# Kernel tuning notes

Measured on AMD Instinct MI355X. Metric: run time of the kernel, lower is better.

Reference implementation:

```python
import jax, jax.numpy as jnp
import numpy as np

B, S, H = 4, 4096, 1024
GAMMA = 0.96875


def decay_mask(seq_len, gamma, dtype=jnp.float32):
    # D[i, j] = gamma**(i-j) for i >= j, else 0 (causal gamma-decay mask)
    i = jnp.arange(seq_len)[:, None]
    j = jnp.arange(seq_len)[None, :]
    exp = (i - j).astype(dtype)
    return jnp.where(i >= j, jnp.power(jnp.asarray(gamma, dtype), exp), jnp.zeros((), dtype))


def setup_inputs() -> dict:
    key = jax.random.key(0)
    ks = jax.random.split(key, 6)
    sc = 1.0 / np.sqrt(H)
    return {
        "x": jax.random.normal(ks[0], (B, S, H), dtype=jnp.float32),
        "Wq": jax.random.normal(ks[1], (H, H), dtype=jnp.float32) * sc,
        "bq": jax.random.normal(ks[2], (H,), dtype=jnp.float32) * 0.01,
        "Wk": jax.random.normal(ks[3], (H, H), dtype=jnp.float32) * sc,
        "bk": jax.random.normal(ks[4], (H,), dtype=jnp.float32) * 0.01,
        "Wv": jax.random.normal(ks[5], (H, H), dtype=jnp.float32) * sc,
    }


def reference(x, Wq, bq, Wk, bk, Wv):
    # Parallel representation of retention.
    seq_len = x.shape[1]
    q = jnp.einsum("bsh,oh->bso", x, Wq) + bq  # [B,S,H]
    k = jnp.einsum("bsh,oh->bso", x, Wk) + bk  # [B,S,H]
    v = jnp.einsum("bsh,oh->bso", x, Wv)       # [B,S,H]
    D = decay_mask(seq_len, GAMMA, x.dtype)     # [S,S]
    scores = jnp.einsum("bqh,bkh->bqk", q, k) * D[None]  # [B,S,S]
    return jnp.einsum("bqk,bkh->bqh", scores, v)
```

## Files before the change

kernel.cpp:

```cpp
#include <hip/hip_runtime.h>


typedef __attribute__((ext_vector_type(8))) short short8;
typedef __attribute__((ext_vector_type(4))) float floatx4;

#define MFMA(a, b, c) __builtin_amdgcn_mfma_f32_16x16x32_bf16((a), (b), (c), 0, 0, 0)

#define B_SZ   4
#define S_LEN  4096
#define H_DIM  1024
#define NROWS  (B_SZ * S_LEN)
#define HP     1088
#define WR     1152
#define LOG2G  (-0.045803690f)

__device__ __forceinline__ unsigned short f32_to_bf16_rn(float f) {
    unsigned int u = __float_as_uint(f);
    u += 0x7FFFu + ((u >> 16) & 1u);
    return (unsigned short)(u >> 16);
}

#define GLOAD_LDS16(gptr, lptr)                                                        \
    __builtin_amdgcn_global_load_lds((__attribute__((address_space(1))) void*)(gptr),  \
                                     (__attribute__((address_space(3))) void*)(lptr),  \
                                     16, 0, 0)

__device__ __forceinline__ void cvt_bf16_body(int i, const float* __restrict__ src,
                                              unsigned short* __restrict__ dst, int n4) {
    if (i >= n4) return;
    float4 v = ((const float4*)src)[i];
    ushort4 o;
    o.x = f32_to_bf16_rn(v.x);
    o.y = f32_to_bf16_rn(v.y);
    o.z = f32_to_bf16_rn(v.z);
    o.w = f32_to_bf16_rn(v.w);
    ((ushort4*)dst)[i] = o;
}

__device__ __forceinline__ void cvt_x_body(int idx, const float* __restrict__ src,
                                           unsigned short* __restrict__ dst) {
    int row = idx >> 7, c8 = (idx & 127) * 8;
    const float4* s = (const float4*)(src + (size_t)row * H_DIM + c8);
    float4 a = s[0], b = s[1];
    ushort4 o0, o1;
    o0.x = f32_to_bf16_rn(a.x); o0.y = f32_to_bf16_rn(a.y);
    o0.z = f32_to_bf16_rn(a.z); o0.w = f32_to_bf16_rn(a.w);
    o1.x = f32_to_bf16_rn(b.x); o1.y = f32_to_bf16_rn(b.y);
    o1.z = f32_to_bf16_rn(b.z); o1.w = f32_to_bf16_rn(b.w);
    ushort4* d = (ushort4*)(dst + (size_t)row * HP + c8);
    d[0] = o0; d[1] = o1;
}

__device__ __forceinline__ void fill_pad_body(int idx, unsigned short* __restrict__ dst) {
    int row = idx >> 3, c = idx & 7;
    uint4 v; v.x = (c == 0) ? 0x00003F80u : 0u; v.y = 0u; v.z = 0u; v.w = 0u;
    *(uint4*)(dst + (size_t)row * HP + 1024 + c * 8) = v;
}

__device__ __forceinline__ void tr_cvt_body(float (&Lt)[128][33],
                                            const float* __restrict__ Wsrc,
                                            const float* __restrict__ bias,
                                            unsigned short* __restrict__ dst,
                                            int bx, int by, int tid) {
    if (by >= 32) {
        if (bx != 0) return;
        const int h0 = by * 32;
#pragma unroll
        for (int i = 0; i < 128; ++i) {
            int idx = i * 256 + tid;
            int r = idx >> 10, cc = idx & 1023;
            int h = h0 + r;
            float v = (h == 1024) ? bias[cc] : 0.0f;
            dst[(size_t)h * 1024 + cc] = f32_to_bf16_rn(v);
        }
        return;
    }
    const int w0 = bx * 128, h0 = by * 32;
#pragma unroll
    for (int i = 0; i < 16; ++i) {
        int idx = i * 256 + tid;
        int r = idx >> 5, cc = idx & 31;
        Lt[r][cc] = Wsrc[(size_t)(w0 + r) * 1024 + h0 + cc];
    }
    __syncthreads();
#pragma unroll
    for (int i = 0; i < 16; ++i) {
        int idx = i * 256 + tid;
        int hh = idx >> 7, ww = idx & 127;
        dst[(size_t)(h0 + hh) * 1024 + w0 + ww] = f32_to_bf16_rn(Lt[ww][hh]);
    }
}

template <int MODE>
__device__ __forceinline__ void gemm_body(unsigned short (&As)[2][128 * 32],
                                          unsigned short (&Bs)[2][128 * 32],
                                          int bx, int by,
                                          const unsigned short* __restrict__ A, int lda,
                                          const unsigned short* __restrict__ W, int ldw,
                                          void* __restrict__ outp, int ldo, int K, int p0) {
    const int tid  = threadIdx.x;
    const int lane = tid & 63;
    const int w4   = tid >> 6;
    const int wm   = w4 >> 1, wn = w4 & 1;
    const int l15  = lane & 15;
    const int q8   = (lane >> 4) * 8;
    const int q4   = (lane >> 4) * 4;

    int aRow0 = 0, wRow0 = 0, kStart = 0;
    const unsigned short* Ap = A;
    const unsigned short* Wp = W;
    const int tT = by;
    const int tl = tT & 31;
    int jt = 0;

    if (MODE == 0) {
        aRow0 = by * 128; wRow0 = bx * 128;
    } else if (MODE == 1) {
        aRow0 = bx * 128; wRow0 = by * 128;
    } else if (MODE == 2) {
        jt = tl - 4 + bx;
        if (jt < 0) return;
        aRow0 = tT * 128;
        wRow0 = (tT >> 5) * S_LEN + jt * 128;
    } else {
        kStart = (tl < 4) ? (4 - tl) * 128 : 0;
        Ap = A + (size_t)tT * 128 * 640;
        Wp = W + (size_t)((tT >> 5) * H_DIM + bx * 128) * S_LEN + (ptrdiff_t)(tl - 4) * 128;
    }

    floatx4 acc[4][4];
#pragma unroll
    for (int i = 0; i < 4; ++i)
#pragma unroll
        for (int j = 0; j < 4; ++j) acc[i][j] = (floatx4)0.0f;

    for (int k0 = kStart; k0 < K; k0 += 64) {
        __syncthreads();
#pragma unroll
        for (int p = 0; p < 2; ++p) {
            const int c = p * 256 + tid;
            const unsigned short* gA = Ap + (size_t)(aRow0 + (c >> 2)) * lda + k0 + (c & 3) * 8;
            const unsigned short* gW = Wp + (size_t)(wRow0 + (c >> 2)) * ldw + k0 + (c & 3) * 8;
            char* dA0 = (char*)&As[0][0] + (size_t)(p * 256 + w4 * 64) * 16;
            char* dA1 = (char*)&As[1][0] + (size_t)(p * 256 + w4 * 64) * 16;
            char* dB0 = (char*)&Bs[0][0] + (size_t)(p * 256 + w4 * 64) * 16;
            char* dB1 = (char*)&Bs[1][0] + (size_t)(p * 256 + w4 * 64) * 16;
            GLOAD_LDS16(gA,      dA0);
            GLOAD_LDS16(gA + 32, dA1);
            GLOAD_LDS16(gW,      dB0);
            GLOAD_LDS16(gW + 32, dB1);
        }
        __syncthreads();

#pragma unroll
        for (int h = 0; h < 2; ++h) {
            short8 af[4], bf[4];
#pragma unroll
            for (int mt = 0; mt < 4; ++mt)
                af[mt] = *(const short8*)(&As[h][0] + (wm * 64 + mt * 16 + l15) * 32 + q8);
#pragma unroll
            for (int nt = 0; nt < 4; ++nt)
                bf[nt] = *(const short8*)(&Bs[h][0] + (wn * 64 + nt * 16 + l15) * 32 + q8);
#pragma unroll
            for (int mt = 0; mt < 4; ++mt)
#pragma unroll
                for (int nt = 0; nt < 4; ++nt)
                    acc[mt][nt] = MFMA(af[mt], bf[nt], acc[mt][nt]);
        }
    }

#pragma unroll
    for (int nt = 0; nt < 4; ++nt) {
        const int ol = wn * 64 + nt * 16 + l15;
#pragma unroll
        for (int mt = 0; mt < 4; ++mt) {
#pragma unroll
            for (int r = 0; r < 4; ++r) {
                const int nl = wm * 64 + mt * 16 + q4 + r;
                const float v = acc[mt][nt][r];
                if (MODE == 0) {
                    const int o = wRow0 + ol;
                    if (o < p0)
                        ((unsigned short*)outp)[(size_t)(aRow0 + nl) * ldo + o] = f32_to_bf16_rn(v);
                } else if (MODE == 1) {
                    const int s = wRow0 + ol;
                    const int hh = aRow0 + nl;
                    ((unsigned short*)outp)[((size_t)(s >> 12) * H_DIM + hh) * S_LEN + (s & (S_LEN - 1))] =
                        f32_to_bf16_rn(v);
                } else if (MODE == 2) {
                    const int d = (tl - jt) * 128 + nl - ol;
                    const float pv = (d >= 0) ? v * exp2f((float)d * LOG2G) : 0.0f;
                    ((unsigned short*)outp)[(size_t)tT * (128 * 640) + (size_t)nl * 640 +
                                            (size_t)bx * 128 + ol] = f32_to_bf16_rn(pv);
                } else {
                    ((float*)outp)[(size_t)(tT * 128 + nl) * H_DIM + bx * 128 + ol] = v;
                }
            }
        }
    }
}

__global__ __launch_bounds__(256) void prep_small(const float* __restrict__ Wq,
                                                  const float* __restrict__ bq,
                                                  const float* __restrict__ Wk,
                                                  const float* __restrict__ bk,
                                                  const float* __restrict__ Wv,
                                                  unsigned short* __restrict__ wqT,
                                                  unsigned short* __restrict__ wkT,
                                                  unsigned short* __restrict__ wvb,
                                                  unsigned short* __restrict__ xtb) {
    __shared__ float Lt[128][33];
    const int t = blockIdx.x, tid = threadIdx.x;
    if (t < 288) {
        tr_cvt_body(Lt, Wq, bq, wqT, t & 7, t >> 3, tid);
    } else if (t < 576) {
        const int t2 = t - 288;
        tr_cvt_body(Lt, Wk, bk, wkT, t2 & 7, t2 >> 3, tid);
    } else if (t < 1600) {
        cvt_bf16_body((t - 576) * 256 + tid, Wv, wvb, H_DIM * H_DIM / 4);
    } else {
        fill_pad_body((t - 1600) * 256 + tid, xtb);
    }
}

__global__ __launch_bounds__(256) void cvtx_p1(const float* __restrict__ x,
                                               unsigned short* __restrict__ xtb,
                                               const unsigned short* __restrict__ wkT,
                                               const unsigned short* __restrict__ wqT,
                                               unsigned short* __restrict__ p1) {
    __shared__ unsigned short As[2][128 * 32];
    __shared__ unsigned short Bs[2][128 * 32];
    const int t = blockIdx.x;
    if (t < 81) {
        gemm_body<0>(As, Bs, t % 9, t / 9, wkT, 1024, wqT, 1024, p1, HP, 1024, HP);
    } else {
        cvt_x_body((t - 81) * 256 + threadIdx.x, x, xtb);
    }
}

__global__ __launch_bounds__(256) void gemm_g(const unsigned short* __restrict__ xtb,
                                              const unsigned short* __restrict__ p1,
                                              unsigned short* __restrict__ gb) {
    __shared__ unsigned short As[2][128 * 32];
    __shared__ unsigned short Bs[2][128 * 32];
    const int bid = blockIdx.x;
    const int g = bid & 7, j = bid >> 3;
    gemm_body<0>(As, Bs, j % 9, g * 16 + j / 9, xtb, HP, p1, HP, gb, HP, HP, HP);
}

__global__ __launch_bounds__(256) void pb_vt(const unsigned short* __restrict__ gb,
                                             const unsigned short* __restrict__ xtb,
                                             const unsigned short* __restrict__ wvb,
                                             unsigned short* __restrict__ pb,
                                             unsigned short* __restrict__ vtb) {
    __shared__ unsigned short As[2][128 * 32];
    __shared__ unsigned short Bs[2][128 * 32];
    const int t = blockIdx.x;
    if (t < 640) {
        const int g = t & 7, j = t >> 3;
        gemm_body<2>(As, Bs, j % 5, g * 16 + j / 5, gb, HP, xtb, HP, pb, 640, HP, 0);
    } else {
        const int t2 = t - 640;
        const int g = t2 & 7, j = t2 >> 3;
        gemm_body<1>(As, Bs, j & 7, g * 16 + (j >> 3), wvb, 1024, xtb, HP, vtb, 0, 1024, 0);
    }
}

__global__ __launch_bounds__(256) void gemm_out(const unsigned short* __restrict__ pb,
                                                const unsigned short* __restrict__ vtb,
                                                float* __restrict__ out) {
    __shared__ unsigned short As[2][128 * 32];
    __shared__ unsigned short Bs[2][128 * 32];
    const int bid = blockIdx.x;
    const int g = bid & 7, j = bid >> 3;
    gemm_body<3>(As, Bs, j & 7, g * 16 + (j >> 3), pb, 640, vtb, S_LEN, out, H_DIM, 640, 0);
}

extern "C" void kernel_launch(void* const* d_in, const int* in_sizes, int n_in,
                              void* d_out, int out_size, void* d_ws, size_t ws_size,
                              hipStream_t stream) {
    (void)in_sizes; (void)n_in; (void)out_size; (void)ws_size;

    const float* x  = (const float*)d_in[0];
    const float* Wq = (const float*)d_in[1];
    const float* bq = (const float*)d_in[2];
    const float* Wk = (const float*)d_in[3];
    const float* bk = (const float*)d_in[4];
    const float* Wv = (const float*)d_in[5];
    float* out = (float*)d_out;

    unsigned short* xtb = (unsigned short*)d_ws;
    unsigned short* gb  = xtb + (size_t)NROWS * HP;
    unsigned short* vtb = gb  + (size_t)NROWS * HP;
    unsigned short* pb  = vtb + (size_t)NROWS * H_DIM;
    unsigned short* wqT = pb  + (size_t)128 * 128 * 640;
    unsigned short* wkT = wqT + (size_t)WR * H_DIM;
    unsigned short* p1  = wkT + (size_t)WR * H_DIM;
    unsigned short* wvb = p1  + (size_t)WR * HP;

    prep_small<<<2112, 256, 0, stream>>>(Wq, bq, Wk, bk, Wv, wqT, wkT, wvb, xtb);
    cvtx_p1<<<81 + 8192, 256, 0, stream>>>(x, xtb, wkT, wqT, p1);
    gemm_g<<<9 * 128, 256, 0, stream>>>(xtb, p1, gb);
    pb_vt<<<640 + 1024, 256, 0, stream>>>(gb, xtb, wvb, pb, vtb);
    gemm_out<<<8 * 128, 256, 0, stream>>>(pb, vtb, out);
}
```

Baseline: 304.3 us.

## Switch main GEMMs to 256x256 tiles with 4-stage async LDS pipeline

Replaces the 128x128 tiles with 256-thread blocks in the three large GEMM stages by 256x256 tiles with 512-thread blocks. Each K step is staged through a 4-deep ring of global-to-LDS async loads using explicit vmcnt waits and barriers, with an XOR swizzle on LDS chunks and raised priority around the MFMA loops. The banded decay-score buffer is re-laid out for 256-wide tiles (768 columns), and unused parts of it are zeroed in the prep kernel. The larger tiles are meant to raise data reuse and hide memory latency. In exchange there are fewer blocks, higher register and LDS pressure, and more wasted work on the causal band.

```diff
diff --git a/kernel.cpp b/kernel.cpp
--- a/kernel.cpp
+++ b/kernel.cpp
@@ -11,7 +11,6 @@
 #define H_DIM  1024
 #define NROWS  (B_SZ * S_LEN)
 #define HP     1088
-#define WR     1152
 #define LOG2G  (-0.045803690f)
 
 __device__ __forceinline__ unsigned short f32_to_bf16_rn(float f) {
@@ -24,6 +23,13 @@
     __builtin_amdgcn_global_load_lds((__attribute__((address_space(1))) void*)(gptr),  \
                                      (__attribute__((address_space(3))) void*)(lptr),  \
                                      16, 0, 0)
+
+#define BAR()                                   \
+    do {                                        \
+        asm volatile("" ::: "memory");          \
+        __builtin_amdgcn_s_barrier();           \
+        asm volatile("" ::: "memory");          \
+    } while (0)
 
 __device__ __forceinline__ void cvt_bf16_body(int i, const float* __restrict__ src,
                                               unsigned short* __restrict__ dst, int n4) {
@@ -57,6 +63,17 @@
     *(uint4*)(dst + (size_t)row * HP + 1024 + c * 8) = v;
 }
 
+__device__ __forceinline__ void zero_pb_body(int idx, unsigned short* __restrict__ pb) {
+    int r = idx >> 13;
+    int rem = idx & 8191;
+    int row = rem >> 5, c8 = (rem & 31) * 8;
+    int batch = r / 3, sub = r % 3;
+    int qt = batch * 16 + (sub == 2 ? 1 : 0);
+    int col0 = (sub == 2 ? 0 : sub * 256);
+    uint4 z; z.x = 0u; z.y = 0u; z.z = 0u; z.w = 0u;
+    *(uint4*)(pb + (size_t)qt * (256 * 768) + (size_t)row * 768 + col0 + c8) = z;
+}
+
 __device__ __forceinline__ void tr_cvt_body(float (&Lt)[128][33],
                                             const float* __restrict__ Wsrc,
                                             const float* __restrict__ bias,
@@ -91,13 +108,13 @@
     }
 }
 
-template <int MODE>
-__device__ __forceinline__ void gemm_body(unsigned short (&As)[2][128 * 32],
-                                          unsigned short (&Bs)[2][128 * 32],
-                                          int bx, int by,
-                                          const unsigned short* __restrict__ A, int lda,
-                                          const unsigned short* __restrict__ W, int ldw,
-                                          void* __restrict__ outp, int ldo, int K, int p0) {
+__device__ __forceinline__ void gemm_body128(unsigned short (&As)[2][128 * 32],
+                                             unsigned short (&Bs)[2][128 * 32],
+                                             int bx, int by,
+                                             const unsigned short* __restrict__ A, int lda,
+                                             const unsigned short* __restrict__ W, int ldw,
+                                             unsigned short* __restrict__ outp, int ldo,
+                                             int K, int p0) {
     const int tid  = threadIdx.x;
     const int lane = tid & 63;
     const int w4   = tid >> 6;
@@ -106,27 +123,7 @@
     const int q8   = (lane >> 4) * 8;
     const int q4   = (lane >> 4) * 4;
 
-    int aRow0 = 0, wRow0 = 0, kStart = 0;
-    const unsigned short* Ap = A;
-    const unsigned short* Wp = W;
-    const int tT = by;
-    const int tl = tT & 31;
-    int jt = 0;
-
-    if (MODE == 0) {
-        aRow0 = by * 128; wRow0 = bx * 128;
-    } else if (MODE == 1) {
-        aRow0 = bx * 128; wRow0 = by * 128;
-    } else if (MODE == 2) {
-        jt = tl - 4 + bx;
-        if (jt < 0) return;
-        aRow0 = tT * 128;
-        wRow0 = (tT >> 5) * S_LEN + jt * 128;
-    } else {
-        kStart = (tl < 4) ? (4 - tl) * 128 : 0;
-        Ap = A + (size_t)tT * 128 * 640;
-        Wp = W + (size_t)((tT >> 5) * H_DIM + bx * 128) * S_LEN + (ptrdiff_t)(tl - 4) * 128;
-    }
+    const int aRow0 = by * 128, wRow0 = bx * 128;
 
     floatx4 acc[4][4];
 #pragma unroll
@@ -134,13 +131,13 @@
 #pragma unroll
         for (int j = 0; j < 4; ++j) acc[i][j] = (floatx4)0.0f;
 
-    for (int k0 = kStart; k0 < K; k0 += 64) {
+    for (int k0 = 0; k0 < K; k0 += 64) {
         __syncthreads();
 #pragma unroll
         for (int p = 0; p < 2; ++p) {
             const int c = p * 256 + tid;
-            const unsigned short* gA = Ap + (size_t)(aRow0 + (c >> 2)) * lda + k0 + (c & 3) * 8;
-            const unsigned short* gW = Wp + (size_t)(wRow0 + (c >> 2)) * ldw + k0 + (c & 3) * 8;
+            const unsigned short* gA = A + (size_t)(aRow0 + (c >> 2)) * lda + k0 + (c & 3) * 8;
+            const unsigned short* gW = W + (size_t)(wRow0 + (c >> 2)) * ldw + k0 + (c & 3) * 8;
             char* dA0 = (char*)&As[0][0] + (size_t)(p * 256 + w4 * 64) * 16;
             char* dA1 = (char*)&As[1][0] + (size_t)(p * 256 + w4 * 64) * 16;
             char* dB0 = (char*)&Bs[0][0] + (size_t)(p * 256 + w4 * 64) * 16;
@@ -177,23 +174,149 @@
 #pragma unroll
             for (int r = 0; r < 4; ++r) {
                 const int nl = wm * 64 + mt * 16 + q4 + r;
+                const int o = wRow0 + ol;
+                if (o < p0)
+                    outp[(size_t)(aRow0 + nl) * ldo + o] = f32_to_bf16_rn(acc[mt][nt][r]);
+            }
+        }
+    }
+}
+
+template <int MODE, int NS>
+__device__ __forceinline__ void g256_body(unsigned short (&lds)[4][2][8192],
+                                          int bx, int by,
+                                          const unsigned short* __restrict__ Abase, int lda,
+                                          const unsigned short* __restrict__ Wbase, int ldw,
+                                          void* __restrict__ outp) {
+    const int tid  = threadIdx.x;
+    const int lane = tid & 63;
+    const int wv   = tid >> 6;
+    const int wm   = wv >> 2, wn = wv & 3;
+    const int l15  = lane & 15;
+    const int q    = lane >> 4;
+    const int q4   = q * 4;
+
+    const unsigned short* Ap;
+    const unsigned short* Wp;
+    int ql = 0;
+    if (MODE == 0) {
+        Ap = Abase + (size_t)(by * 256) * lda;
+        Wp = Wbase + (size_t)(bx * 256) * ldw;
+    } else if (MODE == 1) {
+        Ap = Abase + (size_t)(bx * 256) * lda;
+        Wp = Wbase + (size_t)(by * 256) * ldw;
+    } else if (MODE == 2) {
+        ql = by & 15;
+        const int j256 = ql - 2 + bx;
+        if (j256 < 0) return;
+        Ap = Abase + (size_t)(by * 256) * lda;
+        Wp = Wbase + (size_t)((by >> 4) * S_LEN + j256 * 256) * ldw;
+    } else {
+        ql = by & 15;
+        Ap = Abase + (size_t)by * (256 * 768);
+        Wp = Wbase + ((ptrdiff_t)((by >> 4) * H_DIM + bx * 256)) * S_LEN
+                   + ((ptrdiff_t)ql - 2) * 256;
+    }
+
+    int arow[2], ach[2];
+#pragma unroll
+    for (int i = 0; i < 2; ++i) {
+        int c  = i * 512 + tid;
+        arow[i] = c >> 2;
+        ach[i]  = (((c & 3) ^ ((c >> 3) & 3))) * 8;
+    }
+
+    floatx4 acc[8][4];
+#pragma unroll
+    for (int i = 0; i < 8; ++i)
+#pragma unroll
+        for (int j = 0; j < 4; ++j) acc[i][j] = (floatx4)0.0f;
+
+    auto STAGE = [&](int ks) {
+        const int sl = ks & 3;
+        const int kc = ks * 32;
+        char* da = (char*)&lds[sl][0][0] + (size_t)(wv * 64) * 16;
+        char* db = (char*)&lds[sl][1][0] + (size_t)(wv * 64) * 16;
+#pragma unroll
+        for (int i = 0; i < 2; ++i) {
+            GLOAD_LDS16(Ap + (size_t)arow[i] * lda + kc + ach[i], da + i * 8192);
+            GLOAD_LDS16(Wp + (size_t)arow[i] * ldw + kc + ach[i], db + i * 8192);
+        }
+    };
+
+    auto COMPUTE = [&](int ks) {
+        const int sl = ks & 3;
+        const unsigned short* Asl = &lds[sl][0][0];
+        const unsigned short* Bsl = &lds[sl][1][0];
+        short8 af[8], bf[4];
+#pragma unroll
+        for (int mt = 0; mt < 8; ++mt) {
+            const int row = wm * 128 + mt * 16 + l15;
+            af[mt] = *(const short8*)(Asl + row * 32 + ((q ^ ((row >> 1) & 3)) * 8));
+        }
+#pragma unroll
+        for (int nt = 0; nt < 4; ++nt) {
+            const int row = wn * 64 + nt * 16 + l15;
+            bf[nt] = *(const short8*)(Bsl + row * 32 + ((q ^ ((row >> 1) & 3)) * 8));
+        }
+        __builtin_amdgcn_s_setprio(1);
+#pragma unroll
+        for (int mt = 0; mt < 8; ++mt)
+#pragma unroll
+            for (int nt = 0; nt < 4; ++nt)
+                acc[mt][nt] = MFMA(af[mt], bf[nt], acc[mt][nt]);
+        __builtin_amdgcn_s_setprio(0);
+    };
+
+    STAGE(0); STAGE(1); STAGE(2);
+
+    int ks = 0;
+#pragma unroll 1
+    for (; ks < NS - 3; ++ks) {
+        STAGE(ks + 3);
+        asm volatile("s_waitcnt vmcnt(12)" ::: "memory");
+        BAR();
+        COMPUTE(ks);
+        BAR();
+    }
+    asm volatile("s_waitcnt vmcnt(8)" ::: "memory");
+    BAR();
+    COMPUTE(ks);
+    BAR();
+    asm volatile("s_waitcnt vmcnt(4)" ::: "memory");
+    BAR();
+    COMPUTE(ks + 1);
+    BAR();
+    asm volatile("s_waitcnt vmcnt(0)" ::: "memory");
+    BAR();
+    COMPUTE(ks + 2);
+
+#pragma unroll
+    for (int nt = 0; nt < 4; ++nt) {
+        const int ol = wn * 64 + nt * 16 + l15;
+#pragma unroll
+        for (int mt = 0; mt < 8; ++mt) {
+#pragma unroll
+            for (int r = 0; r < 4; ++r) {
+                const int nl = wm * 128 + mt * 16 + q4 + r;
                 const float v = acc[mt][nt][r];
                 if (MODE == 0) {
-                    const int o = wRow0 + ol;
-                    if (o < p0)
-                        ((unsigned short*)outp)[(size_t)(aRow0 + nl) * ldo + o] = f32_to_bf16_rn(v);
+                    const int o = bx * 256 + ol;
+                    if (o < HP)
+                        ((unsigned short*)outp)[(size_t)(by * 256 + nl) * HP + o] =
+                            f32_to_bf16_rn(v);
                 } else if (MODE == 1) {
-                    const int s = wRow0 + ol;
-                    const int hh = aRow0 + nl;
-                    ((unsigned short*)outp)[((size_t)(s >> 12) * H_DIM + hh) * S_LEN + (s & (S_LEN - 1))] =
-                        f32_to_bf16_rn(v);
+                    const int s  = by * 256 + ol;
+                    const int hh = bx * 256 + nl;
+                    ((unsigned short*)outp)[((size_t)(s >> 12) * H_DIM + hh) * S_LEN +
+                                            (s & (S_LEN - 1))] = f32_to_bf16_rn(v);
                 } else if (MODE == 2) {
-                    const int d = (tl - jt) * 128 + nl - ol;
+                    const int d = (2 - bx) * 256 + nl - ol;
                     const float pv = (d >= 0) ? v * exp2f((float)d * LOG2G) : 0.0f;
-                    ((unsigned short*)outp)[(size_t)tT * (128 * 640) + (size_t)nl * 640 +
-                                            (size_t)bx * 128 + ol] = f32_to_bf16_rn(pv);
+                    ((unsigned short*)outp)[(size_t)by * (256 * 768) + (size_t)nl * 768 +
+                                            bx * 256 + ol] = f32_to_bf16_rn(pv);
                 } else {
-                    ((float*)outp)[(size_t)(tT * 128 + nl) * H_DIM + bx * 128 + ol] = v;
+                    ((float*)outp)[(size_t)(by * 256 + nl) * H_DIM + bx * 256 + ol] = v;
                 }
             }
         }
@@ -208,18 +331,21 @@
                                                   unsigned short* __restrict__ wqT,
                                                   unsigned short* __restrict__ wkT,
                                                   unsigned short* __restrict__ wvb,
+                                                  unsigned short* __restrict__ pb,
                                                   unsigned short* __restrict__ xtb) {
     __shared__ float Lt[128][33];
     const int t = blockIdx.x, tid = threadIdx.x;
     if (t < 288) {
         tr_cvt_body(Lt, Wq, bq, wqT, t & 7, t >> 3, tid);
-    } else if (t < 576) {
+    } else if (t < 608) {
         const int t2 = t - 288;
         tr_cvt_body(Lt, Wk, bk, wkT, t2 & 7, t2 >> 3, tid);
-    } else if (t < 1600) {
-        cvt_bf16_body((t - 576) * 256 + tid, Wv, wvb, H_DIM * H_DIM / 4);
+    } else if (t < 1632) {
+        cvt_bf16_body((t - 608) * 256 + tid, Wv, wvb, H_DIM * H_DIM / 4);
+    } else if (t < 2016) {
+        zero_pb_body((t - 1632) * 256 + tid, pb);
     } else {
-        fill_pad_body((t - 1600) * 256 + tid, xtb);
+        fill_pad_body((t - 2016) * 256 + tid, xtb);
     }
 }
 
@@ -231,49 +357,46 @@
     __shared__ unsigned short As[2][128 * 32];
     __shared__ unsigned short Bs[2][128 * 32];
     const int t = blockIdx.x;
-    if (t < 81) {
-        gemm_body<0>(As, Bs, t % 9, t / 9, wkT, 1024, wqT, 1024, p1, HP, 1024, HP);
+    if (t < 90) {
+        gemm_body128(As, Bs, t % 9, t / 9, wkT, 1024, wqT, 1024, p1, HP, 1024, HP);
     } else {
-        cvt_x_body((t - 81) * 256 + threadIdx.x, x, xtb);
-    }
-}
-
-__global__ __launch_bounds__(256) void gemm_g(const unsigned short* __restrict__ xtb,
-                                              const unsigned short* __restrict__ p1,
-                                              unsigned short* __restrict__ gb) {
-    __shared__ unsigned short As[2][128 * 32];
-    __shared__ unsigned short Bs[2][128 * 32];
+        cvt_x_body((t - 90) * 256 + threadIdx.x, x, xtb);
+    }
+}
+
+__global__ __launch_bounds__(512, 2) void g256_g(const unsigned short* __restrict__ xtb,
+                                                 const unsigned short* __restrict__ p1,
+                                                 unsigned short* __restrict__ gb) {
+    __shared__ unsigned short lds[4][2][8192];
     const int bid = blockIdx.x;
     const int g = bid & 7, j = bid >> 3;
-    gemm_body<0>(As, Bs, j % 9, g * 16 + j / 9, xtb, HP, p1, HP, gb, HP, HP, HP);
-}
-
-__global__ __launch_bounds__(256) void pb_vt(const unsigned short* __restrict__ gb,
-                                             const unsigned short* __restrict__ xtb,
-                                             const unsigned short* __restrict__ wvb,
-                                             unsigned short* __restrict__ pb,
-                                             unsigned short* __restrict__ vtb) {
-    __shared__ unsigned short As[2][128 * 32];
-    __shared__ unsigned short Bs[2][128 * 32];
+    g256_body<0, 34>(lds, j % 5, g * 8 + j / 5, xtb, HP, p1, HP, gb);
+}
+
+__global__ __launch_bounds__(512, 2) void g256_pbvt(const unsigned short* __restrict__ gb,
+                                                    const unsigned short* __restrict__ xtb,
+                                                    const unsigned short* __restrict__ wvb,
+                                                    unsigned short* __restrict__ pb,
+                                                    unsigned short* __restrict__ vtb) {
+    __shared__ unsigned short lds[4][2][8192];
     const int t = blockIdx.x;
-    if (t < 640) {
+    if (t < 192) {
         const int g = t & 7, j = t >> 3;
-        gemm_body<2>(As, Bs, j % 5, g * 16 + j / 5, gb, HP, xtb, HP, pb, 640, HP, 0);
+        g256_body<2, 34>(lds, j % 3, g * 8 + j / 3, gb, HP, xtb, HP, pb);
     } else {
-        const int t2 = t - 640;
+        const int t2 = t - 192;
         const int g = t2 & 7, j = t2 >> 3;
-        gemm_body<1>(As, Bs, j & 7, g * 16 + (j >> 3), wvb, 1024, xtb, HP, vtb, 0, 1024, 0);
-    }
-}
-
-__global__ __launch_bounds__(256) void gemm_out(const unsigned short* __restrict__ pb,
-                                                const unsigned short* __restrict__ vtb,
-                                                float* __restrict__ out) {
-    __shared__ unsigned short As[2][128 * 32];
-    __shared__ unsigned short Bs[2][128 * 32];
+        g256_body<1, 32>(lds, j & 3, g * 8 + (j >> 2), wvb, 1024, xtb, HP, vtb);
+    }
+}
+
+__global__ __launch_bounds__(512, 2) void g256_out(const unsigned short* __restrict__ pb,
+                                                   const unsigned short* __restrict__ vtb,
+                                                   float* __restrict__ out) {
+    __shared__ unsigned short lds[4][2][8192];
     const int bid = blockIdx.x;
     const int g = bid & 7, j = bid >> 3;
-    gemm_body<3>(As, Bs, j & 7, g * 16 + (j >> 3), pb, 640, vtb, S_LEN, out, H_DIM, 640, 0);
+    g256_body<3, 24>(lds, j & 3, g * 8 + (j >> 2), pb, 768, vtb, S_LEN, out);
 }
 
 extern "C" void kernel_launch(void* const* d_in, const int* in_sizes, int n_in,
@@ -293,14 +416,14 @@
     unsigned short* gb  = xtb + (size_t)NROWS * HP;
     unsigned short* vtb = gb  + (size_t)NROWS * HP;
     unsigned short* pb  = vtb + (size_t)NROWS * H_DIM;
-    unsigned short* wqT = pb  + (size_t)128 * 128 * 640;
-    unsigned short* wkT = wqT + (size_t)WR * H_DIM;
-    unsigned short* p1  = wkT + (size_t)WR * H_DIM;
-    unsigned short* wvb = p1  + (size_t)WR * HP;
-
-    prep_small<<<2112, 256, 0, stream>>>(Wq, bq, Wk, bk, Wv, wqT, wkT, wvb, xtb);
-    cvtx_p1<<<81 + 8192, 256, 0, stream>>>(x, xtb, wkT, wqT, p1);
-    gemm_g<<<9 * 128, 256, 0, stream>>>(xtb, p1, gb);
-    pb_vt<<<640 + 1024, 256, 0, stream>>>(gb, xtb, wvb, pb, vtb);
-    gemm_out<<<8 * 128, 256, 0, stream>>>(pb, vtb, out);
-}
+    unsigned short* wqT = pb  + (size_t)64 * 256 * 768;
+    unsigned short* wkT = wqT + (size_t)1152 * 1024;
+    unsigned short* p1  = wkT + (size_t)1280 * 1024;
+    unsigned short* wvb = p1  + (size_t)1280 * HP;
+
+    prep_small<<<2528, 256, 0, stream>>>(Wq, bq, Wk, bk, Wv, wqT, wkT, wvb, pb, xtb);
+    cvtx_p1<<<90 + 8192, 256, 0, stream>>>(x, xtb, wkT, wqT, p1);
+    g256_g<<<320, 512, 0, stream>>>(xtb, p1, gb);
+    g256_pbvt<<<192 + 256, 512, 0, stream>>>(gb, xtb, wvb, pb, vtb);
+    g256_out<<<256, 512, 0, stream>>>(pb, vtb, out);
+}
```

New measurement: 330.3 us. +8.6%, slower.
